# Performance work log

Hardware: AMD Instinct MI355X
Metric: run time of the kernel (lower is better)

## Reference

```python
import jax, jax.numpy as jnp
import numpy as np

B, S, D, H = 4, 2048, 1024, 16
DK = D // H
THETA = 10000.0


def setup_inputs() -> dict:
    key = jax.random.key(0)
    ks = jax.random.split(key, 5)
    std = (2.0 / (D + D)) ** 0.5  # Linear init std (distribution differs from trunc-normal; math identical)
    x = jax.random.normal(ks[0], (B, S, D), dtype=jnp.float32)
    wq = jax.random.normal(ks[1], (D, D), dtype=jnp.float32) * std
    wk = jax.random.normal(ks[2], (D, D), dtype=jnp.float32) * std
    wv = jax.random.normal(ks[3], (D, D), dtype=jnp.float32) * std
    wo = jax.random.normal(ks[4], (D, D), dtype=jnp.float32) * std
    mask = jnp.tril(jnp.ones((S, S), dtype=bool))  # causal
    return {"x": x, "mask": mask, "wq": wq, "wk": wk, "wv": wv, "wo": wo}


def _rope(t):
    # t: [b, h, s, dk]; interleaved pairs (even, odd)
    s = t.shape[-2]
    inv_freq = THETA ** (-jnp.arange(0, DK, 2, dtype=jnp.float32) / DK)  # [dk/2]
    ang = jnp.arange(s, dtype=jnp.float32)[:, None] * inv_freq[None, :]  # [s, dk/2]
    cos = jnp.cos(ang)[None, None, :, :]
    sin = jnp.sin(ang)[None, None, :, :]
    x1 = t[..., 0::2]
    x2 = t[..., 1::2]
    rot = jnp.stack([x1 * cos - x2 * sin, x1 * sin + x2 * cos], axis=-1)
    return rot.reshape(t.shape)


def reference(x, mask, wq, wk, wv, wo):
    b, s, d = x.shape
    def heads(w):
        return jnp.einsum('bsd,ed->bse', x, w).reshape(b, s, H, DK).transpose(0, 2, 1, 3)
    q = _rope(heads(wq))
    k = _rope(heads(wk))
    v = heads(wv)
    scores = jnp.einsum('bhqd,bhkd->bhqk', q, k) / (DK ** 0.5)
    scores = jnp.where(mask, scores, -jnp.inf)
    attn = jax.nn.softmax(scores, axis=-1)
    out = jnp.einsum('bhqk,bhkd->bhqd', attn, v)
    out = out.transpose(0, 2, 1, 3).reshape(b, s, d)
    return jnp.einsum('bsd,ed->bse', out, wo)
```

## Files before the change

### kernel.cpp

```cpp
#include <hip/hip_runtime.h>

constexpr int Bc = 4, Sc = 2048, Dc = 1024, Hc = 16, DKc = 64;
constexpr int Mc = Bc * Sc;

typedef __bf16 bf16x8 __attribute__((ext_vector_type(8)));
typedef float f32x4 __attribute__((ext_vector_type(4)));
typedef unsigned short ush;

#define DEVI __device__ __forceinline__

DEVI ush bf(float f) { return __builtin_bit_cast(ush, (__bf16)f); }

DEVI void ld_lds16(const void* g, void* l) {
    __builtin_amdgcn_global_load_lds(
        (const __attribute__((address_space(1))) unsigned int*)g,
        (__attribute__((address_space(3))) unsigned int*)l,
        16, 0, 0);
}

constexpr unsigned CVT_BLOCKS = 6144;
constexpr unsigned TAB_BLOCKS = 32;

__global__ __launch_bounds__(256) void cvt_all(
    const float* __restrict__ x,  const float* __restrict__ wq,
    const float* __restrict__ wk, const float* __restrict__ wv,
    const float* __restrict__ wo, ush* __restrict__ dst,
    float2* __restrict__ csn)
{
    if (blockIdx.x >= CVT_BLOCKS) {
        int t = (int)(blockIdx.x - CVT_BLOCKS) * 256 + threadIdx.x;
#pragma unroll
        for (int i = 0; i < 8; i++) {
            int idx = t * 8 + i;
            int s = idx >> 5, p = idx & 31;
            float ang = (float)s * exp2f(-(float)p * 0.4152410118609203f);
            csn[idx] = make_float2(cosf(ang), sinf(ang));
        }
        return;
    }
    size_t t = ((size_t)blockIdx.x * 256 + threadIdx.x) * 8;
    const float* src; size_t loc;
    const size_t NX = (size_t)Mc * Dc;
    if (t < NX) { src = x; loc = t; }
    else {
        size_t u = t - NX;
        int wi = (int)(u >> 20);
        src = (wi == 0) ? wq : ((wi == 1) ? wk : ((wi == 2) ? wv : wo));
        loc = u & 1048575u;
    }
    float4 a = *(const float4*)(src + loc);
    float4 b = *(const float4*)(src + loc + 4);
    union { ush u[8]; float4 v; } o;
    o.u[0] = bf(a.x); o.u[1] = bf(a.y); o.u[2] = bf(a.z); o.u[3] = bf(a.w);
    o.u[4] = bf(b.x); o.u[5] = bf(b.y); o.u[6] = bf(b.z); o.u[7] = bf(b.w);
    *(float4*)(dst + t) = o.v;
}

template<int MODE>
__global__ __launch_bounds__(512, 4) void gemm_bf(
    const ush* __restrict__ A,
    const ush* __restrict__ W0, const ush* __restrict__ W1,
    const ush* __restrict__ W2,
    ush* __restrict__ Oq, ush* __restrict__ Ok, ush* __restrict__ Ovt,
    float* __restrict__ Of, const float2* __restrict__ csn)
{
    __shared__ ush sA[128 * 64];
    __shared__ ush sB[128 * 64];

    const int xcd = (int)blockIdx.x;
    const int u = (int)blockIdx.y + 64 * (int)blockIdx.z;
    const int z = (MODE == 0) ? (u >> 6) : 0;
    const int w = u & 63;
    const int m0 = (xcd * 8 + (w >> 3)) * 128;
    const int n0 = (w & 7) * 128;

    const ush* W = (z == 0) ? W0 : ((z == 1) ? W1 : W2);

    const int tid = threadIdx.x;
    const int wv = tid >> 6;
    const int ln = tid & 63;
    const int lr = ln & 15;
    const int lq = ln >> 4;
    const int wm = (wv & 1) * 64;
    const int wn = (wv >> 1) * 32;
    const int rL = ln >> 3;
    const int cSw = ((ln & 7) ^ rL) * 8;
    const int ca0 = lq ^ (ln & 7);

    f32x4 acc[4][2] = {};
    const bool swp = (MODE == 0) && (z == 2);

    for (int kt = 0; kt < 1024; kt += 64) {
        __syncthreads();
#pragma unroll
        for (int i = 0; i < 2; i++) {
            int chunk = wv * 2 + i;
            int rr = chunk * 8 + rL;
            ld_lds16(&A[(size_t)(m0 + rr) * 1024 + kt + cSw], &sA[chunk * 512]);
            ld_lds16(&W[(size_t)(n0 + rr) * 1024 + kt + cSw], &sB[chunk * 512]);
        }
        __syncthreads();
#pragma unroll
        for (int ks = 0; ks < 2; ks++) {
            const int cf = (ca0 ^ (ks << 2)) << 3;
            bf16x8 af[4], bfr[2];
#pragma unroll
            for (int t = 0; t < 4; t++)
                af[t]  = *(const bf16x8*)(&sA[(wm + t * 16 + lr) * 64 + cf]);
#pragma unroll
            for (int t = 0; t < 2; t++)
                bfr[t] = *(const bf16x8*)(&sB[(wn + t * 16 + lr) * 64 + cf]);
            __builtin_amdgcn_s_setprio(1);
            if (!swp) {
#pragma unroll
                for (int ia = 0; ia < 4; ia++)
#pragma unroll
                    for (int ib = 0; ib < 2; ib++)
                        acc[ia][ib] = __builtin_amdgcn_mfma_f32_16x16x32_bf16(
                            af[ia], bfr[ib], acc[ia][ib], 0, 0, 0);
            } else {
#pragma unroll
                for (int ia = 0; ia < 4; ia++)
#pragma unroll
                    for (int ib = 0; ib < 2; ib++)
                        acc[ia][ib] = __builtin_amdgcn_mfma_f32_16x16x32_bf16(
                            bfr[ib], af[ia], acc[ia][ib], 0, 0, 0);
            }
            __builtin_amdgcn_s_setprio(0);
        }
    }

    ush* Oqk = (z == 0) ? Oq : Ok;
#pragma unroll
    for (int ia = 0; ia < 4; ia++) {
#pragma unroll
        for (int ib = 0; ib < 2; ib++) {
#pragma unroll
            for (int r = 0; r < 4; r++) {
                float v = acc[ia][ib][r];
                if (MODE == 1) {
                    int m = m0 + wm + ia * 16 + lq * 4 + r;
                    int n = n0 + wn + ib * 16 + lr;
                    Of[(size_t)m * 1024 + n] = v;
                } else if (swp) {
                    int n = n0 + wn + ib * 16 + lq * 4 + r;
                    int m = m0 + wm + ia * 16 + lr;
                    Ovt[((size_t)((m >> 11) * Hc + (n >> 6)) * DKc + (n & 63)) * Sc
                        + (m & (Sc - 1))] = bf(v);
                } else {
                    int m = m0 + wm + ia * 16 + lq * 4 + r;
                    int n = n0 + wn + ib * 16 + lr;
                    float part = __shfl_xor(v, 1);
                    int dk = n & 63, s = m & (Sc - 1);
                    float2 cs = csn[(s << 5) + (dk >> 1)];
                    float res = (dk & 1) ? (part * cs.y + v * cs.x)
                                         : (v * cs.x - part * cs.y);
                    if (z == 0) res *= 0.18033688011112042f;
                    Oqk[((size_t)((m >> 11) * Hc + (n >> 6)) * Sc + s) * DKc + dk] = bf(res);
                }
            }
        }
    }
}

__global__ __launch_bounds__(512, 4) void attn_k(
    const ush* __restrict__ Q, const ush* __restrict__ Kr,
    const ush* __restrict__ Vt, ush* __restrict__ O)
{
    __shared__ ush kbuf[2][64 * 64];
    __shared__ ush vbuf[2][64 * 64];
    __shared__ ush pbuf[8][16 * 76];

    const int head = (int)blockIdx.x * 8 + ((int)blockIdx.y >> 3);
    const int qp   = (int)blockIdx.y & 7;
    const int tid = threadIdx.x;
    const int wv = tid >> 6;
    const int ln = tid & 63;
    const int lr = ln & 15;
    const int lq = ln >> 4;
    const size_t hoff = (size_t)head * Sc * DKc;
    const int rS = tid >> 3;
    const int c8 = tid & 7;
    const int cS = c8 * 8;
    const int cW = ((c8 ^ (rS & 7)) * 8);
    const int cw0 = ((lq ^ (lr & 7)) * 8);

#define BARRIER() { asm volatile("s_waitcnt lgkmcnt(0)" ::: "memory");       \
        __builtin_amdgcn_sched_barrier(0);                                   \
        __builtin_amdgcn_s_barrier(); }

#define LOADKV(ktv, kk, vv) {                                                \
        int kb_ = (ktv) * 64;                                                \
        kk = *(const float4*)(&Kr[hoff + (size_t)(kb_ + rS) * DKc + cS]);    \
        vv = *(const float4*)(&Vt[hoff + (size_t)rS * Sc + kb_ + cS]); }

#define WRITEKV(bb, kk, vv) {                                                \
        *(float4*)(&kbuf[bb][rS * 64 + cW]) = kk;                            \
        *(float4*)(&vbuf[bb][rS * 64 + cW]) = vv; }

#define COMPUTE(bb, ktv) {                                                   \
        const int kb = (ktv) * 64;                                           \
        if (kb <= qbase + wv * 16 + 15) {       \
        f32x4 sc[4];                                                         \
        __builtin_amdgcn_s_setprio(1);                                       \
        _Pragma("unroll")                                                    \
        for (int nt = 0; nt < 4; nt++) {                                     \
            const ush* kr_ = &kbuf[bb][(nt * 16 + lr) * 64];                 \
            bf16x8 bk0 = *(const bf16x8*)(kr_ + cw0);                        \
            bf16x8 bk1 = *(const bf16x8*)(kr_ + (cw0 ^ 32));                 \
            f32x4 cc = {};                                                   \
                    \
            cc = __builtin_amdgcn_mfma_f32_16x16x32_bf16(bk0, aq0, cc, 0, 0, 0); \
            cc = __builtin_amdgcn_mfma_f32_16x16x32_bf16(bk1, aq1, cc, 0, 0, 0); \
            sc[nt] = cc;                                                     \
        }                                                                    \
        __builtin_amdgcn_s_setprio(0);                                       \
                 \
        const int qg = qbase + wv * 16 + lr;                                 \
        const bool needmask = (kb + 63 > qbase + wv * 16);                   \
        _Pragma("unroll")                                                    \
        for (int nt = 0; nt < 4; nt++) {                                     \
            int k0_ = kb + nt * 16 + lq * 4;                                 \
            _Pragma("unroll")                                                \
            for (int r = 0; r < 4; r++) {                                    \
                float v = sc[nt][r];                                         \
                if (needmask && (k0_ + r) > qg) v = -1e30f;                  \
                float p = exp2f(v);                                          \
                sc[nt][r] = p;                                               \
                rs += p;                                                     \
            }                                                                \
        }                                                                    \
        {                                                                    \
            ush* pb = pbuf[wv];                                              \
                    \
            _Pragma("unroll")                                                \
            for (int nt = 0; nt < 4; nt++) {                                 \
                uint2 u_;                                                    \
                u_.x = (unsigned)bf(sc[nt][0]) | ((unsigned)bf(sc[nt][1]) << 16); \
                u_.y = (unsigned)bf(sc[nt][2]) | ((unsigned)bf(sc[nt][3]) << 16); \
                *(uint2*)(&pb[lr * 76 + nt * 16 + lq * 4]) = u_;             \
            }                                                                \
            __builtin_amdgcn_s_setprio(1);                                   \
            _Pragma("unroll")                                                \
            for (int ks = 0; ks < 2; ks++) {                                 \
                bf16x8 ap = *(const bf16x8*)(&pb[lr * 76 + ks * 32 + lq * 8]); \
                _Pragma("unroll")                                            \
                for (int nt = 0; nt < 4; nt++) {                             \
                    bf16x8 bv = *(const bf16x8*)(&vbuf[bb][(nt * 16 + lr) * 64 \
                                                       + (cw0 ^ (ks * 32))]); \
                    oacc[nt] = __builtin_amdgcn_mfma_f32_16x16x32_bf16(      \
                        ap, bv, oacc[nt], 0, 0, 0);                          \
                }                                                            \
            }                                                                \
            __builtin_amdgcn_s_setprio(0);                                   \
        }                                                                    \
        } }

    for (int half = 0; half < 2; half++) {
        const int qt = half ? (15 - qp) : qp;
        const int qbase = qt * 128;
        const int kmax = 2 * qt + 2;

        bf16x8 aq0, aq1;
        {
            int row = qbase + wv * 16 + lr;
            const ush* qp_ = &Q[hoff + (size_t)row * DKc + lq * 8];
            aq0 = *(const bf16x8*)(qp_);
            aq1 = *(const bf16x8*)(qp_ + 32);
        }

        f32x4 oacc[4] = {};
        float rs = 0.0f;

        float4 ka, va, kb2, vb2;

        LOADKV(0, ka, va);
        WRITEKV(0, ka, va);
        if (kmax > 1) LOADKV(1, kb2, vb2);
        BARRIER();

        int kt = 0;
        while (true) {
            if (kt + 1 < kmax) WRITEKV(1, kb2, vb2);
            if (kt + 2 < kmax) LOADKV(kt + 2, ka, va);
            COMPUTE(0, kt);
            BARRIER();
            kt++;
            if (kt >= kmax) break;
            if (kt + 1 < kmax) WRITEKV(0, ka, va);
            if (kt + 2 < kmax) LOADKV(kt + 2, kb2, vb2);
            COMPUTE(1, kt);
            BARRIER();
            kt++;
            if (kt >= kmax) break;
        }

        const int b = head >> 4, h = head & 15;
        float l = rs;
        l += __shfl_xor(l, 16);
        l += __shfl_xor(l, 32);
#pragma unroll
        for (int r = 0; r < 4; r++) {
            int q = lq * 4 + r;
            float lsum = __shfl(l, (ln & 48) | q);
            float inv = 1.0f / lsum;
            int srow = qbase + wv * 16 + q;
#pragma unroll
            for (int nt = 0; nt < 4; nt++) {
                int e = h * 64 + nt * 16 + lr;
                O[((size_t)(b * Sc + srow)) * Dc + e] = bf(oacc[nt][r] * inv);
            }
        }
    }
#undef BARRIER
#undef LOADKV
#undef WRITEKV
#undef COMPUTE
}

extern "C" void kernel_launch(void* const* d_in, const int* in_sizes, int n_in,
                              void* d_out, int out_size, void* d_ws, size_t ws_size,
                              hipStream_t stream)
{
    (void)in_sizes; (void)n_in; (void)out_size; (void)ws_size;
    const float* x  = (const float*)d_in[0];
    const float* wq = (const float*)d_in[2];
    const float* wk = (const float*)d_in[3];
    const float* wv = (const float*)d_in[4];
    const float* wo = (const float*)d_in[5];

    const size_t N = (size_t)Mc * Dc;
    const size_t NW = (size_t)Dc * Dc;

    ush* xh  = (ush*)d_ws;
    ush* wqh = xh  + N;
    ush* wkh = wqh + NW;
    ush* wvh = wkh + NW;
    ush* woh = wvh + NW;
    ush* vt  = woh + NW;
    ush* ows = vt  + N;
    float2* csn = (float2*)(ows + N);
    ush* qd = (ush*)d_out;
    ush* kd = qd + N;

    cvt_all<<<dim3(CVT_BLOCKS + TAB_BLOCKS), 256, 0, stream>>>(
        x, wq, wk, wv, wo, xh, csn);
    gemm_bf<0><<<dim3(8, 64, 3), 512, 0, stream>>>(
        xh, wqh, wkh, wvh, qd, kd, vt, nullptr, csn);
    attn_k<<<dim3(8, 64), 512, 0, stream>>>(qd, kd, vt, ows);
    gemm_bf<1><<<dim3(8, 64, 1), 512, 0, stream>>>(
        ows, woh, woh, woh, nullptr, nullptr, nullptr, (float*)d_out, csn);
}
```

Before: 275.7 us.

## Load GEMM weight fragments directly into registers, bypassing LDS with prefetch

The GEMM no longer stages the weight tile in shared memory. Each lane now loads its B-operand fragments straight from global memory into registers, double-buffered one K-step ahead. The A tile is still staged through LDS, with manual waitcnt and barrier placement. This halves LDS traffic and footprint per block, which could raise occupancy. The cost is uncoalesced-ish 16-byte global loads of weights that are duplicated across the waves sharing a column range, plus more register pressure.

```diff
diff --git a/kernel.cpp b/kernel.cpp
--- a/kernel.cpp
+++ b/kernel.cpp
@@ -65,7 +65,6 @@
     float* __restrict__ Of, const float2* __restrict__ csn)
 {
     __shared__ ush sA[128 * 64];
-    __shared__ ush sB[128 * 64];
 
     const int xcd = (int)blockIdx.x;
     const int u = (int)blockIdx.y + 64 * (int)blockIdx.z;
@@ -90,45 +89,83 @@
     f32x4 acc[4][2] = {};
     const bool swp = (MODE == 0) && (z == 2);
 
-    for (int kt = 0; kt < 1024; kt += 64) {
-        __syncthreads();
-#pragma unroll
-        for (int i = 0; i < 2; i++) {
-            int chunk = wv * 2 + i;
-            int rr = chunk * 8 + rL;
-            ld_lds16(&A[(size_t)(m0 + rr) * 1024 + kt + cSw], &sA[chunk * 512]);
-            ld_lds16(&W[(size_t)(n0 + rr) * 1024 + kt + cSw], &sB[chunk * 512]);
-        }
-        __syncthreads();
-#pragma unroll
-        for (int ks = 0; ks < 2; ks++) {
-            const int cf = (ca0 ^ (ks << 2)) << 3;
-            bf16x8 af[4], bfr[2];
-#pragma unroll
-            for (int t = 0; t < 4; t++)
-                af[t]  = *(const bf16x8*)(&sA[(wm + t * 16 + lr) * 64 + cf]);
-#pragma unroll
-            for (int t = 0; t < 2; t++)
-                bfr[t] = *(const bf16x8*)(&sB[(wn + t * 16 + lr) * 64 + cf]);
-            __builtin_amdgcn_s_setprio(1);
-            if (!swp) {
-#pragma unroll
-                for (int ia = 0; ia < 4; ia++)
-#pragma unroll
-                    for (int ib = 0; ib < 2; ib++)
-                        acc[ia][ib] = __builtin_amdgcn_mfma_f32_16x16x32_bf16(
-                            af[ia], bfr[ib], acc[ia][ib], 0, 0, 0);
-            } else {
-#pragma unroll
-                for (int ia = 0; ia < 4; ia++)
-#pragma unroll
-                    for (int ib = 0; ib < 2; ib++)
-                        acc[ia][ib] = __builtin_amdgcn_mfma_f32_16x16x32_bf16(
-                            bfr[ib], af[ia], acc[ia][ib], 0, 0, 0);
-            }
-            __builtin_amdgcn_s_setprio(0);
-        }
-    }
+    const ush* Wp0 = &W[(size_t)(n0 + wn + lr) * 1024 + lq * 8];
+    const ush* Wp1 = Wp0 + (size_t)16 * 1024;
+
+#define LOADW(k_, a00, a01, a10, a11) {                                       \
+        a00 = *(const bf16x8*)(Wp0 + (k_));                                   \
+        a01 = *(const bf16x8*)(Wp0 + (k_) + 32);                              \
+        a10 = *(const bf16x8*)(Wp1 + (k_));                                   \
+        a11 = *(const bf16x8*)(Wp1 + (k_) + 32); }
+
+#define STAGE_A(kt_) {                                                        \
+        _Pragma("unroll")                                                     \
+        for (int i = 0; i < 2; i++) {                                         \
+            int chunk = wv * 2 + i;                   \
+            int rr = chunk * 8 + rL;                                          \
+            ld_lds16(&A[(size_t)(m0 + rr) * 1024 + (kt_) + cSw],              \
+                     &sA[chunk * 512]); } }
+
+#define COMPUTE_KS(ksv, b0, b1) {                                             \
+        const int cf = (ca0 ^ ((ksv) << 2)) << 3;                             \
+        bf16x8 af0 = *(const bf16x8*)(&sA[(wm +  0 + lr) * 64 + cf]);         \
+        bf16x8 af1 = *(const bf16x8*)(&sA[(wm + 16 + lr) * 64 + cf]);         \
+        bf16x8 af2 = *(const bf16x8*)(&sA[(wm + 32 + lr) * 64 + cf]);         \
+        bf16x8 af3 = *(const bf16x8*)(&sA[(wm + 48 + lr) * 64 + cf]);         \
+        __builtin_amdgcn_s_setprio(1);                                        \
+        if (!swp) {                                                           \
+            acc[0][0] = __builtin_amdgcn_mfma_f32_16x16x32_bf16(af0, b0, acc[0][0], 0, 0, 0); \
+            acc[0][1] = __builtin_amdgcn_mfma_f32_16x16x32_bf16(af0, b1, acc[0][1], 0, 0, 0); \
+            acc[1][0] = __builtin_amdgcn_mfma_f32_16x16x32_bf16(af1, b0, acc[1][0], 0, 0, 0); \
+            acc[1][1] = __builtin_amdgcn_mfma_f32_16x16x32_bf16(af1, b1, acc[1][1], 0, 0, 0); \
+            acc[2][0] = __builtin_amdgcn_mfma_f32_16x16x32_bf16(af2, b0, acc[2][0], 0, 0, 0); \
+            acc[2][1] = __builtin_amdgcn_mfma_f32_16x16x32_bf16(af2, b1, acc[2][1], 0, 0, 0); \
+            acc[3][0] = __builtin_amdgcn_mfma_f32_16x16x32_bf16(af3, b0, acc[3][0], 0, 0, 0); \
+            acc[3][1] = __builtin_amdgcn_mfma_f32_16x16x32_bf16(af3, b1, acc[3][1], 0, 0, 0); \
+        } else {                                                              \
+            acc[0][0] = __builtin_amdgcn_mfma_f32_16x16x32_bf16(b0, af0, acc[0][0], 0, 0, 0); \
+            acc[0][1] = __builtin_amdgcn_mfma_f32_16x16x32_bf16(b1, af0, acc[0][1], 0, 0, 0); \
+            acc[1][0] = __builtin_amdgcn_mfma_f32_16x16x32_bf16(b0, af1, acc[1][0], 0, 0, 0); \
+            acc[1][1] = __builtin_amdgcn_mfma_f32_16x16x32_bf16(b1, af1, acc[1][1], 0, 0, 0); \
+            acc[2][0] = __builtin_amdgcn_mfma_f32_16x16x32_bf16(b0, af2, acc[2][0], 0, 0, 0); \
+            acc[2][1] = __builtin_amdgcn_mfma_f32_16x16x32_bf16(b1, af2, acc[2][1], 0, 0, 0); \
+            acc[3][0] = __builtin_amdgcn_mfma_f32_16x16x32_bf16(b0, af3, acc[3][0], 0, 0, 0); \
+            acc[3][1] = __builtin_amdgcn_mfma_f32_16x16x32_bf16(b1, af3, acc[3][1], 0, 0, 0); \
+        }                                                                     \
+        __builtin_amdgcn_s_setprio(0); }
+
+    bf16x8 c00, c01, c10, c11, d00, d01, d10, d11;
+    LOADW(0, c00, c01, c10, c11);
+
+    for (int kt = 0; kt < 1024; kt += 128) {
+        STAGE_A(kt);
+        LOADW(kt + 64, d00, d01, d10, d11);
+        asm volatile("s_waitcnt vmcnt(4)" ::: "memory");
+        __builtin_amdgcn_sched_barrier(0);
+        __builtin_amdgcn_s_barrier();
+        COMPUTE_KS(0, c00, c10);
+        COMPUTE_KS(1, c01, c11);
+        asm volatile("s_waitcnt lgkmcnt(0)" ::: "memory");
+        __builtin_amdgcn_sched_barrier(0);
+        __builtin_amdgcn_s_barrier();
+        STAGE_A(kt + 64);
+        if (kt + 128 < 1024) {
+            LOADW(kt + 128, c00, c01, c10, c11);
+            asm volatile("s_waitcnt vmcnt(4)" ::: "memory");
+        } else {
+            asm volatile("s_waitcnt vmcnt(0)" ::: "memory");
+        }
+        __builtin_amdgcn_sched_barrier(0);
+        __builtin_amdgcn_s_barrier();
+        COMPUTE_KS(0, d00, d10);
+        COMPUTE_KS(1, d01, d11);
+        asm volatile("s_waitcnt lgkmcnt(0)" ::: "memory");
+        __builtin_amdgcn_sched_barrier(0);
+        __builtin_amdgcn_s_barrier();
+    }
+#undef LOADW
+#undef STAGE_A
+#undef COMPUTE_KS
 
     ush* Oqk = (z == 0) ? Oq : Ok;
 #pragma unroll
```

New measurement: 350.4 us. 1.27x slower.

## Double-buffer LDS tiles in bf16 GEMM to overlap global loads with MFMA

Applied to the files above, without the earlier changes.

The GEMM main loop now uses two LDS buffers for the A and W tiles, issuing the direct-to-LDS global loads for the next K-step before computing on the current one. This replaces the two barriers per K-step with a single vmcnt wait plus barrier. The aim is to hide global-load latency behind the matrix-core work. In exchange the kernel doubles LDS use to 64 KB per block, which may cut occupancy below the four blocks per CU that the launch bounds request.

```diff
diff --git a/kernel.cpp b/kernel.cpp
--- a/kernel.cpp
+++ b/kernel.cpp
@@ -64,8 +64,8 @@
     ush* __restrict__ Oq, ush* __restrict__ Ok, ush* __restrict__ Ovt,
     float* __restrict__ Of, const float2* __restrict__ csn)
 {
-    __shared__ ush sA[128 * 64];
-    __shared__ ush sB[128 * 64];
+    __shared__ ush sA[2][128 * 64];
+    __shared__ ush sB[2][128 * 64];
 
     const int xcd = (int)blockIdx.x;
     const int u = (int)blockIdx.y + 64 * (int)blockIdx.z;
@@ -90,45 +90,67 @@
     f32x4 acc[4][2] = {};
     const bool swp = (MODE == 0) && (z == 2);
 
-    for (int kt = 0; kt < 1024; kt += 64) {
-        __syncthreads();
-#pragma unroll
-        for (int i = 0; i < 2; i++) {
-            int chunk = wv * 2 + i;
-            int rr = chunk * 8 + rL;
-            ld_lds16(&A[(size_t)(m0 + rr) * 1024 + kt + cSw], &sA[chunk * 512]);
-            ld_lds16(&W[(size_t)(n0 + rr) * 1024 + kt + cSw], &sB[chunk * 512]);
-        }
-        __syncthreads();
-#pragma unroll
-        for (int ks = 0; ks < 2; ks++) {
-            const int cf = (ca0 ^ (ks << 2)) << 3;
-            bf16x8 af[4], bfr[2];
-#pragma unroll
-            for (int t = 0; t < 4; t++)
-                af[t]  = *(const bf16x8*)(&sA[(wm + t * 16 + lr) * 64 + cf]);
-#pragma unroll
-            for (int t = 0; t < 2; t++)
-                bfr[t] = *(const bf16x8*)(&sB[(wn + t * 16 + lr) * 64 + cf]);
-            __builtin_amdgcn_s_setprio(1);
-            if (!swp) {
-#pragma unroll
-                for (int ia = 0; ia < 4; ia++)
-#pragma unroll
-                    for (int ib = 0; ib < 2; ib++)
-                        acc[ia][ib] = __builtin_amdgcn_mfma_f32_16x16x32_bf16(
-                            af[ia], bfr[ib], acc[ia][ib], 0, 0, 0);
-            } else {
-#pragma unroll
-                for (int ia = 0; ia < 4; ia++)
-#pragma unroll
-                    for (int ib = 0; ib < 2; ib++)
-                        acc[ia][ib] = __builtin_amdgcn_mfma_f32_16x16x32_bf16(
-                            bfr[ib], af[ia], acc[ia][ib], 0, 0, 0);
-            }
-            __builtin_amdgcn_s_setprio(0);
-        }
-    }
+#define STAGE(buf, kt_) {                                                     \
+        _Pragma("unroll")                                                     \
+        for (int i = 0; i < 2; i++) {                                         \
+            int chunk = wv * 2 + i;                   \
+            int rr = chunk * 8 + rL;                                          \
+            ld_lds16(&A[(size_t)(m0 + rr) * 1024 + (kt_) + cSw],              \
+                     &sA[buf][chunk * 512]);                                  \
+            ld_lds16(&W[(size_t)(n0 + rr) * 1024 + (kt_) + cSw],              \
+                     &sB[buf][chunk * 512]);                                  \
+        } }
+
+#define COMPUTE(b) {                                                          \
+        const ush* pA = sA[b]; const ush* pB = sB[b];                         \
+        _Pragma("unroll")                                                     \
+        for (int ks = 0; ks < 2; ks++) {                                      \
+            const int cf = (ca0 ^ (ks << 2)) << 3;                            \
+            bf16x8 af[4], bfr[2];                                             \
+            _Pragma("unroll")                                                 \
+            for (int t = 0; t < 4; t++)                                       \
+                af[t]  = *(const bf16x8*)(&pA[(wm + t * 16 + lr) * 64 + cf]); \
+            _Pragma("unroll")                                                 \
+            for (int t = 0; t < 2; t++)                                       \
+                bfr[t] = *(const bf16x8*)(&pB[(wn + t * 16 + lr) * 64 + cf]); \
+            __builtin_amdgcn_s_setprio(1);                                    \
+            if (!swp) {                                                       \
+                _Pragma("unroll")                                             \
+                for (int ia = 0; ia < 4; ia++)                                \
+                    _Pragma("unroll")                                         \
+                    for (int ib = 0; ib < 2; ib++)                            \
+                        acc[ia][ib] = __builtin_amdgcn_mfma_f32_16x16x32_bf16(\
+                            af[ia], bfr[ib], acc[ia][ib], 0, 0, 0);           \
+            } else {                                                          \
+                _Pragma("unroll")                                             \
+                for (int ia = 0; ia < 4; ia++)                                \
+                    _Pragma("unroll")                                         \
+                    for (int ib = 0; ib < 2; ib++)                            \
+                        acc[ia][ib] = __builtin_amdgcn_mfma_f32_16x16x32_bf16(\
+                            bfr[ib], af[ia], acc[ia][ib], 0, 0, 0);           \
+            }                                                                 \
+            __builtin_amdgcn_s_setprio(0);                                    \
+        } }
+
+#define STEP_END() {                                                          \
+        asm volatile("s_waitcnt vmcnt(0)" ::: "memory");                      \
+        __builtin_amdgcn_sched_barrier(0);                                    \
+        __builtin_amdgcn_s_barrier(); }
+
+    STAGE(0, 0);
+    STEP_END();
+
+    for (int kt = 0; kt < 1024; kt += 128) {
+        STAGE(1, kt + 64);
+        COMPUTE(0);
+        STEP_END();
+        if (kt + 128 < 1024) STAGE(0, kt + 128);
+        COMPUTE(1);
+        STEP_END();
+    }
+#undef STAGE
+#undef COMPUTE
+#undef STEP_END
 
     ush* Oqk = (z == 0) ? Oq : Ok;
 #pragma unroll
```

Result: no change. 273.6 us (-0.8%).
